# Kernel optimization log

Hardware: AMD Instinct MI355X
Metric: run time of the kernel (lower is better)

Reference implementation:

```python
import jax, jax.numpy as jnp
import numpy as np

D_MODEL = 1024
N_HEADS = 16
D_K = D_MODEL // N_HEADS


def setup_inputs() -> dict:
    key = jax.random.key(0)
    k1, k2, k3 = jax.random.split(key, 3)
    x = jax.random.normal(k1, (4, 2048, D_MODEL), dtype=jnp.float32)
    # torch nn.Linear(d, 3d, bias=False): y = x @ W.T ; we store W.T directly as (in, out)
    w_qkv = jax.random.normal(k2, (D_MODEL, 3 * D_MODEL), dtype=jnp.float32) * (1.0 / np.sqrt(D_MODEL))
    w_out = jax.random.normal(k3, (D_MODEL, D_MODEL), dtype=jnp.float32) * (1.0 / np.sqrt(D_MODEL))
    return {"x": x, "w_qkv": w_qkv, "w_out": w_out}


def reference(x, w_qkv, w_out):
    B, T, D = x.shape
    qkv = jnp.einsum('btd,de->bte', x, w_qkv)  # (B,T,3D)
    q, k, v = jnp.split(qkv, 3, axis=-1)
    # split heads -> (B,H,T,d_k)
    def split_heads(t):
        return t.reshape(B, T, N_HEADS, D_K).transpose(0, 2, 1, 3)
    q, k, v = split_heads(q), split_heads(k), split_heads(v)
    scale = 1.0 / np.sqrt(D_K).astype(np.float32)
    scores = jnp.einsum('bhqd,bhkd->bhqk', q, k) * scale  # (B,H,T,T)
    causal = jnp.triu(jnp.full((T, T), -jnp.inf, dtype=scores.dtype), k=1)
    scores = scores + causal[None, None]
    weights = jax.nn.softmax(scores, axis=-1)
    attn = jnp.einsum('bhqk,bhkd->bhqd', weights, v)
    attn = attn.transpose(0, 2, 1, 3).reshape(B, T, D)
    return jnp.einsum('btd,de->bte', attn, w_out)
```

## Files before the change

kernel.cpp:

```cpp
#include <hip/hip_runtime.h>
#include <hip/hip_bf16.h>

typedef short short8 __attribute__((ext_vector_type(8)));
typedef float f32x4 __attribute__((ext_vector_type(4)));
typedef float f32x16 __attribute__((ext_vector_type(16)));

#define MFMA16(a, b, c) __builtin_amdgcn_mfma_f32_16x16x32_bf16((a), (b), (c), 0, 0, 0)
#define MFMA32(a, b, c) __builtin_amdgcn_mfma_f32_32x32x16_bf16((a), (b), (c), 0, 0, 0)

#define GLOAD16(gp, lp)                                                    \
    __builtin_amdgcn_global_load_lds(                                      \
        (const __attribute__((address_space(1))) unsigned int*)(gp),       \
        (__attribute__((address_space(3))) unsigned int*)(lp), 16, 0, 0)

__device__ __forceinline__ unsigned short f2b(float x) {
    unsigned int u = __float_as_uint(x);
    unsigned int r = u + 0x7FFFu + ((u >> 16) & 1u);
    return (unsigned short)(r >> 16);
}

#if __has_builtin(__builtin_amdgcn_cvt_pk_bf16_f32)
__device__ __forceinline__ unsigned pack2(float a, float b) {
    auto v = __builtin_amdgcn_cvt_pk_bf16_f32(a, b);
    unsigned u;
    __builtin_memcpy(&u, &v, 4);
    return u;
}
#else
__device__ __forceinline__ unsigned pack2(float a, float b) {
    return (unsigned)f2b(a) | ((unsigned)f2b(b) << 16);
}
#endif

__global__ __launch_bounds__(256) void cast4_kernel(const float* __restrict__ in,
                                                    unsigned short* __restrict__ out,
                                                    int n4) {
    int i = blockIdx.x * 256 + threadIdx.x;
    if (i < n4) {
        float4 v = ((const float4*)in)[i];
        ushort4 o;
        o.x = f2b(v.x); o.y = f2b(v.y); o.z = f2b(v.z); o.w = f2b(v.w);
        ((ushort4*)out)[i] = o;
    }
}

__global__ __launch_bounds__(256) void transpose_cast_f32(const float* __restrict__ in,
                                                          unsigned short* __restrict__ out,
                                                          int K, int N) {
    __shared__ unsigned short Ls[64 * 66];
    const int k0 = blockIdx.y * 64, n0 = blockIdx.x * 64;
    const int tid = threadIdx.x;
    const int krow = tid >> 4, nc4 = (tid & 15) * 4;
#pragma unroll
    for (int p = 0; p < 4; p++) {
        float4 v = *(const float4*)(in + (size_t)(k0 + krow + p * 16) * N + n0 + nc4);
        unsigned* d32 = (unsigned*)(Ls + (krow + p * 16) * 66 + nc4);
        d32[0] = pack2(v.x, v.y);
        d32[1] = pack2(v.z, v.w);
    }
    __syncthreads();
    const int n = tid >> 3, kc = (tid & 7) * 8;
#pragma unroll
    for (int p = 0; p < 2; p++) {
        int nn = n + p * 32;
        unsigned short w[8];
#pragma unroll
        for (int j = 0; j < 8; j++) w[j] = Ls[(kc + j) * 66 + nn];
        *(short8*)(out + (size_t)(n0 + nn) * K + k0 + kc) = *(short8*)w;
    }
}

__global__ __launch_bounds__(512, 2) void gemm_qk(const unsigned short* __restrict__ A,
                                                  const unsigned short* __restrict__ Bt,
                                                  unsigned short* __restrict__ Qb,
                                                  unsigned short* __restrict__ Kb) {
    __shared__ __align__(16) unsigned short smem[65536];

    const int tid  = threadIdx.x;
    const int wave = tid >> 6;
    const int lane = tid & 63;
    const int l32  = lane & 31;
    const int hi   = lane >> 5;
    const int wr   = wave >> 2;
    const int wc   = wave & 3;

    const int bid = blockIdx.x;
    const int sid = (bid & 7) * 32 + (bid >> 3);
    const int bx  = sid & 7;
    const int by  = sid >> 3;
    const int m0 = by * 256;
    const int n0 = bx * 256;

    const int srow = tid >> 3;
    const int cswz = (((tid & 7) ^ ((tid >> 3) & 7)) * 8);
    const unsigned short* gA = A  + (size_t)(m0 + srow) * 1024 + cswz;
    const unsigned short* gB = Bt + (size_t)(n0 + srow) * 1024 + cswz;

#define STAGE_A(buf, h, kt) do {                                              \
        const unsigned short* _g = gA + (size_t)((h) * 128) * 1024 + (kt) * 64; \
        unsigned short* _l = smem + (buf) * 16384 + (h) * 8192 + wave * 512;  \
        GLOAD16(_g, _l);                                                      \
        GLOAD16(_g + 65536, _l + 4096);                                       \
    } while (0)
#define STAGE_B(buf, h, kt) do {                                              \
        const unsigned short* _g = gB + (size_t)((h) * 128) * 1024 + (kt) * 64; \
        unsigned short* _l = smem + 32768 + (buf) * 16384 + (h) * 8192 + wave * 512; \
        GLOAD16(_g, _l);                                                      \
        GLOAD16(_g + 65536, _l + 4096);                                       \
    } while (0)

    const int sw7  = l32 & 7;
    const int aoff = (wr * 128 + l32) * 64;
    const int boff = (wc * 64 + l32) * 64;

    f32x16 acc[4][2] = {};

    STAGE_A(0, 0, 0); STAGE_A(0, 1, 0); STAGE_B(0, 0, 0); STAGE_B(0, 1, 0);
    STAGE_B(1, 0, 1); STAGE_B(1, 1, 1); STAGE_A(1, 0, 1);
    asm volatile("s_waitcnt vmcnt(6)" ::: "memory");
    __builtin_amdgcn_s_barrier();

#pragma unroll
    for (int t = 0; t < 16; ++t) {
        const int b = t & 1;
        const unsigned short* Ab = smem + b * 16384;
        const unsigned short* Bb = smem + 32768 + b * 16384;

        short8 afLo[2][4], afHi[2][4], bf0[4], bf1[4];

#pragma unroll
        for (int rf = 0; rf < 2; ++rf)
#pragma unroll
            for (int ks = 0; ks < 4; ++ks)
                afLo[rf][ks] = *(const short8*)(Ab + aoff + rf * 2048 + (((ks * 2 + hi) ^ sw7) * 8));
#pragma unroll
        for (int ks = 0; ks < 4; ++ks)
            bf0[ks] = *(const short8*)(Bb + boff + (((ks * 2 + hi) ^ sw7) * 8));
        if (t + 1 < 16) STAGE_A(b ^ 1, 1, t + 1);
        __builtin_amdgcn_s_barrier();
        asm volatile("s_waitcnt lgkmcnt(0)" ::: "memory");
        __builtin_amdgcn_s_setprio(1);
#pragma unroll
        for (int ks = 0; ks < 4; ++ks) {
            acc[0][0] = MFMA32(bf0[ks], afLo[0][ks], acc[0][0]);
            acc[1][0] = MFMA32(bf0[ks], afLo[1][ks], acc[1][0]);
        }
        __builtin_amdgcn_s_setprio(0);
        __builtin_amdgcn_s_barrier();

#pragma unroll
        for (int ks = 0; ks < 4; ++ks)
            bf1[ks] = *(const short8*)(Bb + boff + 2048 + (((ks * 2 + hi) ^ sw7) * 8));
        __builtin_amdgcn_s_barrier();
        asm volatile("s_waitcnt lgkmcnt(0)" ::: "memory");
        __builtin_amdgcn_s_setprio(1);
#pragma unroll
        for (int ks = 0; ks < 4; ++ks) {
            acc[0][1] = MFMA32(bf1[ks], afLo[0][ks], acc[0][1]);
            acc[1][1] = MFMA32(bf1[ks], afLo[1][ks], acc[1][1]);
        }
        __builtin_amdgcn_s_setprio(0);
        __builtin_amdgcn_s_barrier();

#pragma unroll
        for (int rf = 0; rf < 2; ++rf)
#pragma unroll
            for (int ks = 0; ks < 4; ++ks)
                afHi[rf][ks] = *(const short8*)(Ab + aoff + (2 + rf) * 2048 + (((ks * 2 + hi) ^ sw7) * 8));
        if (t + 2 < 16) { STAGE_B(b, 0, t + 2); STAGE_B(b, 1, t + 2); }
        __builtin_amdgcn_s_barrier();
        asm volatile("s_waitcnt lgkmcnt(0)" ::: "memory");
        __builtin_amdgcn_s_setprio(1);
#pragma unroll
        for (int ks = 0; ks < 4; ++ks) {
            acc[2][0] = MFMA32(bf0[ks], afHi[0][ks], acc[2][0]);
            acc[3][0] = MFMA32(bf0[ks], afHi[1][ks], acc[3][0]);
        }
        __builtin_amdgcn_s_setprio(0);
        __builtin_amdgcn_s_barrier();

        if (t + 2 < 16) {
            STAGE_A(b, 0, t + 2);
            asm volatile("s_waitcnt vmcnt(6)" ::: "memory");
        } else {
            asm volatile("s_waitcnt vmcnt(0)" ::: "memory");
        }
        __builtin_amdgcn_s_barrier();
        __builtin_amdgcn_s_setprio(1);
#pragma unroll
        for (int ks = 0; ks < 4; ++ks) {
            acc[2][1] = MFMA32(bf1[ks], afHi[0][ks], acc[2][1]);
            acc[3][1] = MFMA32(bf1[ks], afHi[1][ks], acc[3][1]);
        }
        __builtin_amdgcn_s_setprio(0);
        __builtin_amdgcn_s_barrier();
    }
#undef STAGE_A
#undef STAGE_B

    unsigned short* outp = (n0 < 1024) ? Qb : Kb;
    const int cb = (n0 < 1024) ? n0 : n0 - 1024;
    const float QS = (n0 < 1024) ? 0.125f * 1.44269504f : 1.0f;
#pragma unroll
    for (int rf = 0; rf < 4; ++rf) {
        const int row = m0 + wr * 128 + rf * 32 + l32;
#pragma unroll
        for (int cf = 0; cf < 2; ++cf)
#pragma unroll
            for (int g = 0; g < 4; ++g) {
                const int col = cb + wc * 64 + cf * 32 + g * 8 + 4 * hi;
                uint2 v;
                v.x = pack2(acc[rf][cf][4 * g + 0] * QS, acc[rf][cf][4 * g + 1] * QS);
                v.y = pack2(acc[rf][cf][4 * g + 2] * QS, acc[rf][cf][4 * g + 3] * QS);
                *(uint2*)(outp + (size_t)row * 1024 + col) = v;
            }
    }
}

__global__ __launch_bounds__(512, 2) void gemm_v(const unsigned short* __restrict__ A,
                                                 const unsigned short* __restrict__ Bt,
                                                 unsigned short* __restrict__ Vt) {
    __shared__ __align__(16) unsigned short smem[49152];

    const int tid  = threadIdx.x;
    const int wave = tid >> 6;
    const int lane = tid & 63;
    const int l32  = lane & 31;
    const int hi   = lane >> 5;
    const int wr   = wave >> 2;
    const int wc   = wave & 3;

    const int bid = blockIdx.x;
    const int sid = (bid & 7) * 32 + (bid >> 3);
    const int bx  = sid & 3;
    const int by  = sid >> 2;
    const int m0 = by * 128;
    const int n0 = bx * 256;

    const int srow = tid >> 3;
    const int cswz = (((tid & 7) ^ ((tid >> 3) & 7)) * 8);
    const unsigned short* gA = A  + (size_t)(m0 + srow) * 1024 + cswz;
    const unsigned short* gB = Bt + (size_t)(n0 + srow) * 1024 + cswz;

#define STAGE_A(buf, h, kt) do {                                              \
        const unsigned short* _g = gA + (size_t)((h) * 64) * 1024 + (kt) * 64; \
        unsigned short* _l = smem + (buf) * 8192 + (h) * 4096 + wave * 512;   \
        GLOAD16(_g, _l);                                                      \
    } while (0)
#define STAGE_B(buf, h, kt) do {                                              \
        const unsigned short* _g = gB + (size_t)((h) * 128) * 1024 + (kt) * 64; \
        unsigned short* _l = smem + 16384 + (buf) * 16384 + (h) * 8192 + wave * 512; \
        GLOAD16(_g, _l);                                                      \
        GLOAD16(_g + 65536, _l + 4096);                                       \
    } while (0)

    const int sw7  = l32 & 7;
    const int aoff = (wr * 64 + l32) * 64;
    const int boff = (wc * 64 + l32) * 64;

    f32x16 acc[2][2] = {};

    STAGE_A(0, 0, 0); STAGE_A(0, 1, 0); STAGE_B(0, 0, 0); STAGE_B(0, 1, 0);
    STAGE_B(1, 0, 1); STAGE_B(1, 1, 1); STAGE_A(1, 0, 1);
    asm volatile("s_waitcnt vmcnt(5)" ::: "memory");
    __builtin_amdgcn_s_barrier();

#pragma unroll
    for (int t = 0; t < 16; ++t) {
        const int b = t & 1;
        const unsigned short* Ab = smem + b * 8192;
        const unsigned short* Bb = smem + 16384 + b * 16384;

        short8 af0[4], af1[4], bf0[4], bf1[4];

#pragma unroll
        for (int ks = 0; ks < 4; ++ks)
            af0[ks] = *(const short8*)(Ab + aoff + (((ks * 2 + hi) ^ sw7) * 8));
#pragma unroll
        for (int ks = 0; ks < 4; ++ks)
            bf0[ks] = *(const short8*)(Bb + boff + (((ks * 2 + hi) ^ sw7) * 8));
        if (t + 1 < 16) STAGE_A(b ^ 1, 1, t + 1);
        __builtin_amdgcn_s_barrier();
        asm volatile("s_waitcnt lgkmcnt(0)" ::: "memory");
        __builtin_amdgcn_s_setprio(1);
#pragma unroll
        for (int ks = 0; ks < 4; ++ks)
            acc[0][0] = MFMA32(af0[ks], bf0[ks], acc[0][0]);
        __builtin_amdgcn_s_setprio(0);
        __builtin_amdgcn_s_barrier();

#pragma unroll
        for (int ks = 0; ks < 4; ++ks)
            bf1[ks] = *(const short8*)(Bb + boff + 2048 + (((ks * 2 + hi) ^ sw7) * 8));
        __builtin_amdgcn_s_barrier();
        asm volatile("s_waitcnt lgkmcnt(0)" ::: "memory");
        __builtin_amdgcn_s_setprio(1);
#pragma unroll
        for (int ks = 0; ks < 4; ++ks)
            acc[0][1] = MFMA32(af0[ks], bf1[ks], acc[0][1]);
        __builtin_amdgcn_s_setprio(0);
        __builtin_amdgcn_s_barrier();

#pragma unroll
        for (int ks = 0; ks < 4; ++ks)
            af1[ks] = *(const short8*)(Ab + aoff + 2048 + (((ks * 2 + hi) ^ sw7) * 8));
        if (t + 2 < 16) { STAGE_B(b, 0, t + 2); STAGE_B(b, 1, t + 2); }
        __builtin_amdgcn_s_barrier();
        asm volatile("s_waitcnt lgkmcnt(0)" ::: "memory");
        __builtin_amdgcn_s_setprio(1);
#pragma unroll
        for (int ks = 0; ks < 4; ++ks)
            acc[1][0] = MFMA32(af1[ks], bf0[ks], acc[1][0]);
        __builtin_amdgcn_s_setprio(0);
        __builtin_amdgcn_s_barrier();

        if (t + 2 < 16) {
            STAGE_A(b, 0, t + 2);
            asm volatile("s_waitcnt vmcnt(5)" ::: "memory");
        } else {
            asm volatile("s_waitcnt vmcnt(0)" ::: "memory");
        }
        __builtin_amdgcn_s_barrier();
        __builtin_amdgcn_s_setprio(1);
#pragma unroll
        for (int ks = 0; ks < 4; ++ks)
            acc[1][1] = MFMA32(af1[ks], bf1[ks], acc[1][1]);
        __builtin_amdgcn_s_setprio(0);
        __builtin_amdgcn_s_barrier();
    }
#undef STAGE_A
#undef STAGE_B

    const int bb = m0 >> 11, t0b = m0 & 2047;
    const int hbase = n0 >> 6;
    unsigned short* reg = smem + wc * 8192;
#pragma unroll
    for (int rf = 0; rf < 2; ++rf)
#pragma unroll
        for (int cf = 0; cf < 2; ++cf)
#pragma unroll
            for (int rg = 0; rg < 4; ++rg) {
                const int tl = wr * 64 + rf * 32 + rg * 8 + 4 * hi;
                const int d  = cf * 32 + l32;
                const int w  = d * 64 + ((tl >> 1) ^ (4 * (d & 7)));
                uint2 v;
                v.x = pack2(acc[rf][cf][4 * rg + 0], acc[rf][cf][4 * rg + 1]);
                v.y = pack2(acc[rf][cf][4 * rg + 2], acc[rf][cf][4 * rg + 3]);
                *(uint2*)(reg + 2 * w) = v;
            }
    __syncthreads();
#pragma unroll
    for (int it = 0; it < 8; ++it) {
        const int id = it * 512 + tid;
        const int hh = id >> 10, d = (id >> 4) & 63, k = id & 15;
        const int kb = k >> 2, kl = k & 3;
        const int xx = 4 * (d & 7);
        const unsigned short* bp = smem + hh * 8192 + 2 * (d * 64);
        uint2 lo  = *(const uint2*)(bp + 2 * ((16 * kb + 2 * kl) ^ xx));
        uint2 hi2 = *(const uint2*)(bp + 2 * ((16 * kb + 2 * kl + 8) ^ xx));
        uint2 parts[2] = {lo, hi2};
        short8 v; __builtin_memcpy(&v, parts, 16);
        *(short8*)(Vt + ((size_t)((bb * 16 + hbase + hh) * 64 + d)) * 2048 + t0b + k * 8) = v;
    }
}

__global__ __launch_bounds__(512, 2) void gemm_out(const unsigned short* __restrict__ A,
                                                   const unsigned short* __restrict__ Bt,
                                                   float* __restrict__ C) {
    __shared__ __align__(16) unsigned short smem[49152];

    const int tid  = threadIdx.x;
    const int wave = tid >> 6;
    const int lane = tid & 63;
    const int l32  = lane & 31;
    const int hi   = lane >> 5;
    const int wr   = wave >> 2;
    const int wc   = wave & 3;

    const int bid = blockIdx.x;
    const int sid = (bid & 7) * 32 + (bid >> 3);
    const int bx  = sid & 3;
    const int by  = sid >> 2;
    const int m0 = by * 128;
    const int n0 = bx * 256;

    const int srow = tid >> 3;
    const int cswz = (((tid & 7) ^ ((tid >> 3) & 7)) * 8);
    const unsigned short* gA = A  + (size_t)(m0 + srow) * 1024 + cswz;
    const unsigned short* gB = Bt + (size_t)(n0 + srow) * 1024 + cswz;

#define STAGE_A(buf, h, kt) do {                                              \
        const unsigned short* _g = gA + (size_t)((h) * 64) * 1024 + (kt) * 64; \
        unsigned short* _l = smem + (buf) * 8192 + (h) * 4096 + wave * 512;   \
        GLOAD16(_g, _l);                                                      \
    } while (0)
#define STAGE_B(buf, h, kt) do {                                              \
        const unsigned short* _g = gB + (size_t)((h) * 128) * 1024 + (kt) * 64; \
        unsigned short* _l = smem + 16384 + (buf) * 16384 + (h) * 8192 + wave * 512; \
        GLOAD16(_g, _l);                                                      \
        GLOAD16(_g + 65536, _l + 4096);                                       \
    } while (0)

    const int sw7  = l32 & 7;
    const int aoff = (wr * 64 + l32) * 64;
    const int boff = (wc * 64 + l32) * 64;

    f32x16 acc[2][2] = {};

    STAGE_A(0, 0, 0); STAGE_A(0, 1, 0); STAGE_B(0, 0, 0); STAGE_B(0, 1, 0);
    STAGE_B(1, 0, 1); STAGE_B(1, 1, 1); STAGE_A(1, 0, 1);
    asm volatile("s_waitcnt vmcnt(5)" ::: "memory");
    __builtin_amdgcn_s_barrier();

#pragma unroll
    for (int t = 0; t < 16; ++t) {
        const int b = t & 1;
        const unsigned short* Ab = smem + b * 8192;
        const unsigned short* Bb = smem + 16384 + b * 16384;

        short8 af0[4], af1[4], bf0[4], bf1[4];

#pragma unroll
        for (int ks = 0; ks < 4; ++ks)
            af0[ks] = *(const short8*)(Ab + aoff + (((ks * 2 + hi) ^ sw7) * 8));
#pragma unroll
        for (int ks = 0; ks < 4; ++ks)
            bf0[ks] = *(const short8*)(Bb + boff + (((ks * 2 + hi) ^ sw7) * 8));
        if (t + 1 < 16) STAGE_A(b ^ 1, 1, t + 1);
        __builtin_amdgcn_s_barrier();
        asm volatile("s_waitcnt lgkmcnt(0)" ::: "memory");
        __builtin_amdgcn_s_setprio(1);
#pragma unroll
        for (int ks = 0; ks < 4; ++ks)
            acc[0][0] = MFMA32(af0[ks], bf0[ks], acc[0][0]);
        __builtin_amdgcn_s_setprio(0);
        __builtin_amdgcn_s_barrier();

#pragma unroll
        for (int ks = 0; ks < 4; ++ks)
            bf1[ks] = *(const short8*)(Bb + boff + 2048 + (((ks * 2 + hi) ^ sw7) * 8));
        __builtin_amdgcn_s_barrier();
        asm volatile("s_waitcnt lgkmcnt(0)" ::: "memory");
        __builtin_amdgcn_s_setprio(1);
#pragma unroll
        for (int ks = 0; ks < 4; ++ks)
            acc[0][1] = MFMA32(af0[ks], bf1[ks], acc[0][1]);
        __builtin_amdgcn_s_setprio(0);
        __builtin_amdgcn_s_barrier();

#pragma unroll
        for (int ks = 0; ks < 4; ++ks)
            af1[ks] = *(const short8*)(Ab + aoff + 2048 + (((ks * 2 + hi) ^ sw7) * 8));
        if (t + 2 < 16) { STAGE_B(b, 0, t + 2); STAGE_B(b, 1, t + 2); }
        __builtin_amdgcn_s_barrier();
        asm volatile("s_waitcnt lgkmcnt(0)" ::: "memory");
        __builtin_amdgcn_s_setprio(1);
#pragma unroll
        for (int ks = 0; ks < 4; ++ks)
            acc[1][0] = MFMA32(af1[ks], bf0[ks], acc[1][0]);
        __builtin_amdgcn_s_setprio(0);
        __builtin_amdgcn_s_barrier();

        if (t + 2 < 16) {
            STAGE_A(b, 0, t + 2);
            asm volatile("s_waitcnt vmcnt(5)" ::: "memory");
        } else {
            asm volatile("s_waitcnt vmcnt(0)" ::: "memory");
        }
        __builtin_amdgcn_s_barrier();
        __builtin_amdgcn_s_setprio(1);
#pragma unroll
        for (int ks = 0; ks < 4; ++ks)
            acc[1][1] = MFMA32(af1[ks], bf1[ks], acc[1][1]);
        __builtin_amdgcn_s_setprio(0);
        __builtin_amdgcn_s_barrier();
    }
#undef STAGE_A
#undef STAGE_B

#pragma unroll
    for (int rf = 0; rf < 2; ++rf)
#pragma unroll
        for (int cf = 0; cf < 2; ++cf)
#pragma unroll
            for (int r = 0; r < 16; ++r) {
                int row = m0 + wr * 64 + rf * 32 + (r & 3) + 8 * (r >> 2) + 4 * hi;
                int col = n0 + wc * 64 + cf * 32 + l32;
                C[(size_t)row * 1024 + col] = acc[rf][cf][r];
            }
}

__global__ __launch_bounds__(512, 4) void attention_kernel(const unsigned short* Qb,
                                                           const unsigned short* Kb,
                                                           const unsigned short* Vt,
                                                           unsigned short* attn) {
    const int T = 2048;
    const int bi = blockIdx.x;
    const int pp = bi >> 6;
    const int hb = bi & 63;
    const int b = hb >> 4, h = hb & 15;
    const int tid = threadIdx.x, wave = tid >> 6, lane = tid & 63;
    const int l16 = lane & 15, quad = lane >> 4;

    const unsigned short* Qp  = Qb + (size_t)b * T * 1024 + h * 64;
    const unsigned short* Kp  = Kb + (size_t)b * T * 1024 + h * 64;
    const unsigned short* Vbh = Vt + ((size_t)(b * 16 + h) * 64) * 2048;

    __shared__ __align__(16) unsigned short smem[2][16384];

    const f32x4 fz = {};
    short8 onesf;
#pragma unroll
    for (int e = 0; e < 8; e++) onesf[e] = (short)0x3F80;

    const int srow = lane >> 2;
    const int scol = (((lane & 3) ^ ((lane >> 3) & 3)) * 8);
    const int sw8  = ((l16 >> 1) & 3) * 8;

    const unsigned short* gs;
    size_t ktstep, jstep;
    int lofs;
    if (wave < 4) {
        const int p = wave >> 1, cp = wave & 1;
        gs = Kp + (size_t)(cp * 32 + srow) * 1024 + p * 32 + scol;
        ktstep = (size_t)64 * 1024; jstep = (size_t)16 * 1024;
        lofs = p * 2048 + cp * 1024;
    } else {
        const int u = wave - 4, th = u >> 1, cp = u & 1;
        gs = Vbh + (size_t)(cp * 32 + srow) * 2048 + th * 32 + scol;
        ktstep = (size_t)64; jstep = (size_t)16 * 2048;
        lofs = 4096 + th * 2048 + cp * 1024;
    }

#define STAGE(bb, k64, sub) do {                               \
        const unsigned short* _g = gs + (size_t)(k64) * ktstep; \
        unsigned short* _l = &smem[bb][0] + (sub) * 8192 + lofs; \
        GLOAD16(_g, _l);                                        \
        GLOAD16(_g + jstep, _l + 512);                          \
    } while (0)

    for (int pass = 0; pass < 2; ++pass) {
        const int qb = pass ? pp : (15 - pp);
        const int qw0 = qb * 128 + wave * 16;

        short8 qf[2];
#pragma unroll
        for (int kd = 0; kd < 2; kd++)
            qf[kd] = *(const short8*)(Qp + (size_t)(qw0 + l16) * 1024 + kd * 32 + quad * 8);
        asm volatile("" ::: "memory");

        f32x4 o[4] = {};
        f32x4 o_l = {};

        STAGE(0, 0, 0); STAGE(0, 1, 1);
        const int last = qb;
        for (int kt = 0; kt <= last; kt++) {
            const int bsel = kt & 1;
            if (kt < last) {
                STAGE(bsel ^ 1, 2 * (kt + 1), 0);
                STAGE(bsel ^ 1, 2 * (kt + 1) + 1, 1);
                asm volatile("s_waitcnt vmcnt(4)" ::: "memory");
            } else {
                asm volatile("s_waitcnt vmcnt(0)" ::: "memory");
            }
            __builtin_amdgcn_s_barrier();
            asm volatile("" ::: "memory");

#pragma unroll
            for (int sub = 0; sub < 2; ++sub) {
                const int tk0 = kt * 128 + sub * 64;
                const unsigned short* Kb0 = &smem[bsel][sub * 8192];
                const unsigned short* Kb1 = Kb0 + 2048;
                const unsigned short* Vb0 = Kb0 + 4096;

#pragma unroll
                for (int th = 0; th < 2; th++) {
                    const int t0a = tk0 + th * 32;
                    if (t0a > qw0 + 15) continue;
                    const int t1 = t0a + 16;
                    const bool act1 = (t1 <= qw0 + 15);

                    f32x4 s0, s1;
                    {
                        const int row = (th * 2) * 16 + l16;
                        short8 kf0 = *(const short8*)(Kb0 + row * 32 + (quad * 8 ^ sw8));
                        short8 kf1 = *(const short8*)(Kb1 + row * 32 + (quad * 8 ^ sw8));
                        s0 = MFMA16(kf0, qf[0], fz);
                        s0 = MFMA16(kf1, qf[1], s0);
                    }
                    if (act1) {
                        const int row = (th * 2 + 1) * 16 + l16;
                        short8 kf0 = *(const short8*)(Kb0 + row * 32 + (quad * 8 ^ sw8));
                        short8 kf1 = *(const short8*)(Kb1 + row * 32 + (quad * 8 ^ sw8));
                        s1 = MFMA16(kf0, qf[0], fz);
                        s1 = MFMA16(kf1, qf[1], s1);
                    }

                    unsigned u00, u01, u10, u11;
                    {
                        const bool full = (t0a + 15) <= qw0;
                        float p[4];
#pragma unroll
                        for (int r = 0; r < 4; r++) {
                            float e = __builtin_amdgcn_exp2f(s0[r]);
                            if (!full)
                                e = (t0a + quad * 4 + r <= qw0 + l16) ? e : 0.f;
                            p[r] = e;
                        }
                        u00 = pack2(p[0], p[1]);
                        u01 = pack2(p[2], p[3]);
                    }
                    if (act1) {
                        const bool full = (t1 + 15) <= qw0;
                        float p[4];
#pragma unroll
                        for (int r = 0; r < 4; r++) {
                            float e = __builtin_amdgcn_exp2f(s1[r]);
                            if (!full)
                                e = (t1 + quad * 4 + r <= qw0 + l16) ? e : 0.f;
                            p[r] = e;
                        }
                        u10 = pack2(p[0], p[1]);
                        u11 = pack2(p[2], p[3]);
                    } else {
                        u10 = 0; u11 = 0;
                    }

                    unsigned pb[4] = {u00, u01, u10, u11};
                    short8 pf; __builtin_memcpy(&pf, pb, 16);

                    __builtin_amdgcn_s_setprio(1);
                    o_l = MFMA16(onesf, pf, o_l);
#pragma unroll
                    for (int dt = 0; dt < 4; dt++) {
                        short8 vf = *(const short8*)(Vb0 + th * 2048 + (dt * 16 + l16) * 32 + (quad * 8 ^ sw8));
                        o[dt] = MFMA16(vf, pf, o[dt]);
                    }
                    __builtin_amdgcn_s_setprio(0);
                }
            }
            asm volatile("" ::: "memory");
            __builtin_amdgcn_s_barrier();
        }

        const float rl = 1.f / o_l[0];
        const int q = qw0 + l16;
#pragma unroll
        for (int dt = 0; dt < 4; dt++) {
            ushort4 wv;
            wv.x = f2b(o[dt][0] * rl);
            wv.y = f2b(o[dt][1] * rl);
            wv.z = f2b(o[dt][2] * rl);
            wv.w = f2b(o[dt][3] * rl);
            *(ushort4*)(attn + (size_t)(b * T + q) * 1024 + h * 64 + dt * 16 + quad * 4) = wv;
        }
    }
#undef STAGE
}

extern "C" void kernel_launch(void* const* d_in, const int* in_sizes, int n_in,
                              void* d_out, int out_size, void* d_ws, size_t ws_size,
                              hipStream_t stream) {
    const float* x     = (const float*)d_in[0];
    const float* w_qkv = (const float*)d_in[1];
    const float* w_out = (const float*)d_in[2];
    float* out = (float*)d_out;

    const int M = 8192, D = 1024, E = 3072;
    const size_t MB = 1048576;

    char* ws = (char*)d_ws;
    unsigned short* xb    = (unsigned short*)ws;
    unsigned short* wqkvT = (unsigned short*)(ws + 16 * MB);
    unsigned short* woutT = (unsigned short*)(ws + 22 * MB);
    unsigned short* Qb    = (unsigned short*)(ws + 24 * MB);
    unsigned short* Kb    = (unsigned short*)(ws + 40 * MB);
    unsigned short* Vt    = (unsigned short*)(ws + 56 * MB);

    cast4_kernel<<<M * D / 4 / 256, 256, 0, stream>>>(x, xb, M * D / 4);
    transpose_cast_f32<<<dim3(E / 64, D / 64), 256, 0, stream>>>(w_qkv, wqkvT, D, E);
    transpose_cast_f32<<<dim3(D / 64, D / 64), 256, 0, stream>>>(w_out, woutT, D, D);

    gemm_qk<<<dim3(256), 512, 0, stream>>>(xb, wqkvT, Qb, Kb);
    gemm_v<<<dim3(256), 512, 0, stream>>>(xb, wqkvT + (size_t)2048 * 1024, Vt);

    attention_kernel<<<dim3(512), 512, 0, stream>>>(Qb, Kb, Vt, Qb);

    gemm_out<<<dim3(256), 512, 0, stream>>>(Qb, woutT, out);
}
```

Before: 243.8 us.

## Halve attention block to 4 waves, each computing two 16-row query tiles

The attention kernel now launches 256 threads (4 waves) instead of 8, and each wave processes two 16-row query tiles (A and B, 64 rows apart). Each K and V fragment read from LDS therefore feeds twice as many MFMAs. Each staging wave issues four global-to-LDS loads per stage instead of two, and the wait count is adjusted to match. This cuts LDS read traffic and per-block load-issue overhead, but raises register pressure and the causal-mask branching per wave. It also leaves fewer waves per block to hide latency, since the launch bound drops to (256,2).

```diff
diff --git a/kernel.cpp b/kernel.cpp
--- a/kernel.cpp
+++ b/kernel.cpp
@@ -490,7 +490,7 @@
             }
 }
 
-__global__ __launch_bounds__(512, 4) void attention_kernel(const unsigned short* Qb,
+__global__ __launch_bounds__(256, 2) void attention_kernel(const unsigned short* Qb,
                                                            const unsigned short* Kb,
                                                            const unsigned short* Vt,
                                                            unsigned short* attn) {
@@ -517,40 +517,44 @@
     const int scol = (((lane & 3) ^ ((lane >> 3) & 3)) * 8);
     const int sw8  = ((l16 >> 1) & 3) * 8;
 
-    const unsigned short* gs;
-    size_t ktstep, jstep;
+    const unsigned short* gs0;
+    size_t ktstep, rstep;
     int lofs;
-    if (wave < 4) {
-        const int p = wave >> 1, cp = wave & 1;
-        gs = Kp + (size_t)(cp * 32 + srow) * 1024 + p * 32 + scol;
-        ktstep = (size_t)64 * 1024; jstep = (size_t)16 * 1024;
-        lofs = p * 2048 + cp * 1024;
+    if (wave < 2) {
+        gs0 = Kp + (size_t)srow * 1024 + wave * 32 + scol;
+        ktstep = (size_t)64 * 1024; rstep = 1024;
+        lofs = wave * 2048;
     } else {
-        const int u = wave - 4, th = u >> 1, cp = u & 1;
-        gs = Vbh + (size_t)(cp * 32 + srow) * 2048 + th * 32 + scol;
-        ktstep = (size_t)64; jstep = (size_t)16 * 2048;
-        lofs = 4096 + th * 2048 + cp * 1024;
-    }
-
-#define STAGE(bb, k64, sub) do {                               \
-        const unsigned short* _g = gs + (size_t)(k64) * ktstep; \
-        unsigned short* _l = &smem[bb][0] + (sub) * 8192 + lofs; \
-        GLOAD16(_g, _l);                                        \
-        GLOAD16(_g + jstep, _l + 512);                          \
+        const int th = wave - 2;
+        gs0 = Vbh + (size_t)srow * 2048 + th * 32 + scol;
+        ktstep = (size_t)64; rstep = 2048;
+        lofs = 4096 + th * 2048;
+    }
+
+#define STAGE(bb, k64, sub) do {                                  \
+        const unsigned short* _g = gs0 + (size_t)(k64) * ktstep;  \
+        unsigned short* _l = &smem[bb][0] + (sub) * 8192 + lofs;  \
+        GLOAD16(_g,              _l);                             \
+        GLOAD16(_g + 16 * rstep, _l + 512);                       \
+        GLOAD16(_g + 32 * rstep, _l + 1024);                      \
+        GLOAD16(_g + 48 * rstep, _l + 1536);                      \
     } while (0)
 
     for (int pass = 0; pass < 2; ++pass) {
         const int qb = pass ? pp : (15 - pp);
-        const int qw0 = qb * 128 + wave * 16;
-
-        short8 qf[2];
-#pragma unroll
-        for (int kd = 0; kd < 2; kd++)
-            qf[kd] = *(const short8*)(Qp + (size_t)(qw0 + l16) * 1024 + kd * 32 + quad * 8);
+        const int qw0A = qb * 128 + wave * 16;
+        const int qw0B = qw0A + 64;
+
+        short8 qfA[2], qfB[2];
+#pragma unroll
+        for (int kd = 0; kd < 2; kd++) {
+            qfA[kd] = *(const short8*)(Qp + (size_t)(qw0A + l16) * 1024 + kd * 32 + quad * 8);
+            qfB[kd] = *(const short8*)(Qp + (size_t)(qw0B + l16) * 1024 + kd * 32 + quad * 8);
+        }
         asm volatile("" ::: "memory");
 
-        f32x4 o[4] = {};
-        f32x4 o_l = {};
+        f32x4 oA[4] = {}, oB[4] = {};
+        f32x4 olA = {}, olB = {};
 
         STAGE(0, 0, 0); STAGE(0, 1, 1);
         const int last = qb;
@@ -559,7 +563,7 @@
             if (kt < last) {
                 STAGE(bsel ^ 1, 2 * (kt + 1), 0);
                 STAGE(bsel ^ 1, 2 * (kt + 1) + 1, 1);
-                asm volatile("s_waitcnt vmcnt(4)" ::: "memory");
+                asm volatile("s_waitcnt vmcnt(8)" ::: "memory");
             } else {
                 asm volatile("s_waitcnt vmcnt(0)" ::: "memory");
             }
@@ -576,65 +580,106 @@
 #pragma unroll
                 for (int th = 0; th < 2; th++) {
                     const int t0a = tk0 + th * 32;
-                    if (t0a > qw0 + 15) continue;
+                    if (t0a > qw0B + 15) continue;
                     const int t1 = t0a + 16;
-                    const bool act1 = (t1 <= qw0 + 15);
-
-                    f32x4 s0, s1;
+                    const bool actA  = (t0a <= qw0A + 15);
+                    const bool act1B = (t1 <= qw0B + 15);
+                    const bool act1A = (t1 <= qw0A + 15);
+
+                    f32x4 s0A, s0B, s1A, s1B;
                     {
                         const int row = (th * 2) * 16 + l16;
                         short8 kf0 = *(const short8*)(Kb0 + row * 32 + (quad * 8 ^ sw8));
                         short8 kf1 = *(const short8*)(Kb1 + row * 32 + (quad * 8 ^ sw8));
-                        s0 = MFMA16(kf0, qf[0], fz);
-                        s0 = MFMA16(kf1, qf[1], s0);
+                        s0B = MFMA16(kf0, qfB[0], fz);
+                        s0B = MFMA16(kf1, qfB[1], s0B);
+                        if (actA) {
+                            s0A = MFMA16(kf0, qfA[0], fz);
+                            s0A = MFMA16(kf1, qfA[1], s0A);
+                        }
                     }
-                    if (act1) {
+                    if (act1B) {
                         const int row = (th * 2 + 1) * 16 + l16;
                         short8 kf0 = *(const short8*)(Kb0 + row * 32 + (quad * 8 ^ sw8));
                         short8 kf1 = *(const short8*)(Kb1 + row * 32 + (quad * 8 ^ sw8));
-                        s1 = MFMA16(kf0, qf[0], fz);
-                        s1 = MFMA16(kf1, qf[1], s1);
+                        s1B = MFMA16(kf0, qfB[0], fz);
+                        s1B = MFMA16(kf1, qfB[1], s1B);
+                        if (act1A) {
+                            s1A = MFMA16(kf0, qfA[0], fz);
+                            s1A = MFMA16(kf1, qfA[1], s1A);
+                        }
                     }
 
-                    unsigned u00, u01, u10, u11;
+                    unsigned uB0, uB1, uB2, uB3;
                     {
-                        const bool full = (t0a + 15) <= qw0;
+                        const bool full = (t0a + 15) <= qw0B;
                         float p[4];
 #pragma unroll
                         for (int r = 0; r < 4; r++) {
-                            float e = __builtin_amdgcn_exp2f(s0[r]);
+                            float e = __builtin_amdgcn_exp2f(s0B[r]);
                             if (!full)
-                                e = (t0a + quad * 4 + r <= qw0 + l16) ? e : 0.f;
+                                e = (t0a + quad * 4 + r <= qw0B + l16) ? e : 0.f;
                             p[r] = e;
                         }
-                        u00 = pack2(p[0], p[1]);
-                        u01 = pack2(p[2], p[3]);
+                        uB0 = pack2(p[0], p[1]);
+                        uB1 = pack2(p[2], p[3]);
                     }
-                    if (act1) {
-                        const bool full = (t1 + 15) <= qw0;
+                    if (act1B) {
+                        const bool full = (t1 + 15) <= qw0B;
                         float p[4];
 #pragma unroll
                         for (int r = 0; r < 4; r++) {
-                            float e = __builtin_amdgcn_exp2f(s1[r]);
+                            float e = __builtin_amdgcn_exp2f(s1B[r]);
                             if (!full)
-                                e = (t1 + quad * 4 + r <= qw0 + l16) ? e : 0.f;
+                                e = (t1 + quad * 4 + r <= qw0B + l16) ? e : 0.f;
                             p[r] = e;
                         }
-                        u10 = pack2(p[0], p[1]);
-                        u11 = pack2(p[2], p[3]);
+                        uB2 = pack2(p[0], p[1]);
+                        uB3 = pack2(p[2], p[3]);
                     } else {
-                        u10 = 0; u11 = 0;
+                        uB2 = 0; uB3 = 0;
                     }
-
-                    unsigned pb[4] = {u00, u01, u10, u11};
-                    short8 pf; __builtin_memcpy(&pf, pb, 16);
+                    unsigned uA0 = 0, uA1 = 0, uA2 = 0, uA3 = 0;
+                    if (actA) {
+                        const bool full = (t0a + 15) <= qw0A;
+                        float p[4];
+#pragma unroll
+                        for (int r = 0; r < 4; r++) {
+                            float e = __builtin_amdgcn_exp2f(s0A[r]);
+                            if (!full)
+                                e = (t0a + quad * 4 + r <= qw0A + l16) ? e : 0.f;
+                            p[r] = e;
+                        }
+                        uA0 = pack2(p[0], p[1]);
+                        uA1 = pack2(p[2], p[3]);
+                        if (act1A) {
+                            const bool fullH = (t1 + 15) <= qw0A;
+                            float q[4];
+#pragma unroll
+                            for (int r = 0; r < 4; r++) {
+                                float e = __builtin_amdgcn_exp2f(s1A[r]);
+                                if (!fullH)
+                                    e = (t1 + quad * 4 + r <= qw0A + l16) ? e : 0.f;
+                                q[r] = e;
+                            }
+                            uA2 = pack2(q[0], q[1]);
+                            uA3 = pack2(q[2], q[3]);
+                        }
+                    }
+
+                    unsigned pbB[4] = {uB0, uB1, uB2, uB3};
+                    short8 pfB; __builtin_memcpy(&pfB, pbB, 16);
+                    unsigned pbA[4] = {uA0, uA1, uA2, uA3};
+                    short8 pfA; __builtin_memcpy(&pfA, pbA, 16);
 
                     __builtin_amdgcn_s_setprio(1);
-                    o_l = MFMA16(onesf, pf, o_l);
+                    olB = MFMA16(onesf, pfB, olB);
+                    if (actA) olA = MFMA16(onesf, pfA, olA);
 #pragma unroll
                     for (int dt = 0; dt < 4; dt++) {
                         short8 vf = *(const short8*)(Vb0 + th * 2048 + (dt * 16 + l16) * 32 + (quad * 8 ^ sw8));
-                        o[dt] = MFMA16(vf, pf, o[dt]);
+                        oB[dt] = MFMA16(vf, pfB, oB[dt]);
+                        if (actA) oA[dt] = MFMA16(vf, pfA, oA[dt]);
                     }
                     __builtin_amdgcn_s_setprio(0);
                 }
@@ -643,16 +688,26 @@
             __builtin_amdgcn_s_barrier();
         }
 
-        const float rl = 1.f / o_l[0];
-        const int q = qw0 + l16;
-#pragma unroll
-        for (int dt = 0; dt < 4; dt++) {
-            ushort4 wv;
-            wv.x = f2b(o[dt][0] * rl);
-            wv.y = f2b(o[dt][1] * rl);
-            wv.z = f2b(o[dt][2] * rl);
-            wv.w = f2b(o[dt][3] * rl);
-            *(ushort4*)(attn + (size_t)(b * T + q) * 1024 + h * 64 + dt * 16 + quad * 4) = wv;
+        {
+            const float rlA = 1.f / olA[0];
+            const float rlB = 1.f / olB[0];
+            const int qA = qw0A + l16;
+            const int qB = qw0B + l16;
+#pragma unroll
+            for (int dt = 0; dt < 4; dt++) {
+                ushort4 wv;
+                wv.x = f2b(oA[dt][0] * rlA);
+                wv.y = f2b(oA[dt][1] * rlA);
+                wv.z = f2b(oA[dt][2] * rlA);
+                wv.w = f2b(oA[dt][3] * rlA);
+                *(ushort4*)(attn + (size_t)(b * T + qA) * 1024 + h * 64 + dt * 16 + quad * 4) = wv;
+                ushort4 wv2;
+                wv2.x = f2b(oB[dt][0] * rlB);
+                wv2.y = f2b(oB[dt][1] * rlB);
+                wv2.z = f2b(oB[dt][2] * rlB);
+                wv2.w = f2b(oB[dt][3] * rlB);
+                *(ushort4*)(attn + (size_t)(b * T + qB) * 1024 + h * 64 + dt * 16 + quad * 4) = wv2;
+            }
         }
     }
 #undef STAGE
@@ -684,7 +739,7 @@
     gemm_qk<<<dim3(256), 512, 0, stream>>>(xb, wqkvT, Qb, Kb);
     gemm_v<<<dim3(256), 512, 0, stream>>>(xb, wqkvT + (size_t)2048 * 1024, Vt);
 
-    attention_kernel<<<dim3(512), 512, 0, stream>>>(Qb, Kb, Vt, Qb);
+    attention_kernel<<<dim3(512), 256, 0, stream>>>(Qb, Kb, Vt, Qb);
 
     gemm_out<<<dim3(256), 512, 0, stream>>>(Qb, woutT, out);
 }
```

After: 269.8 us. +10.7%, slower.
